# Performance work log

Hardware: AMD Instinct MI355X
Metric: run time of the kernel (lower is better)

Reference implementation:

```python
import jax, jax.numpy as jnp
import numpy as np

B, H, W, C = 8, 64, 64, 512   # C = query_dim = text_dim
K = 256                        # text tokens
TOP_M = 5
EPS = 1e-5


def _ln(x, g, b):
    mu = jnp.mean(x, axis=-1, keepdims=True)
    var = jnp.var(x, axis=-1, keepdims=True)
    return (x - mu) / jnp.sqrt(var + EPS) * g + b


def setup_inputs() -> dict:
    key = jax.random.key(0)
    ks = jax.random.split(key, 10)
    s = 0.02
    return {
        "visual": jax.random.normal(ks[0], (B, H, W, C), jnp.float32),
        "text": jax.random.normal(ks[1], (B, K, C), jnp.float32),
        "g1": jnp.ones((C,), jnp.float32), "b1": jnp.zeros((C,), jnp.float32),
        "g2": jnp.ones((C,), jnp.float32), "b2": jnp.zeros((C,), jnp.float32),
        "Wq": jax.random.normal(ks[2], (C, C), jnp.float32) * s,   # query_dim -> text_dim
        "Wv": jax.random.normal(ks[3], (C, C), jnp.float32) * s,   # text_dim -> query_dim
        "logit_scale": jnp.asarray(np.log(1.0 / 0.07), jnp.float32),
        "Wg": jax.random.normal(ks[4], (C, 1), jnp.float32) * s,
        "bg": jnp.zeros((1,), jnp.float32),
        "W1": jax.random.normal(ks[5], (C, 4 * C), jnp.float32) * s,
        "bff1": jnp.zeros((4 * C,), jnp.float32),
        "W2": jax.random.normal(ks[6], (4 * C, C), jnp.float32) * s,
        "bff2": jnp.zeros((C,), jnp.float32),
    }


def reference(visual, text, g1, b1, g2, b2, Wq, Wv, logit_scale, Wg, bg, W1, bff1, W2, bff2):
    Bv, Hv, Wdim, Cv = visual.shape
    N = Hv * Wdim
    x = _ln(visual, g1, b1).reshape(Bv, N, Cv)           # (B,N,C) pre-LN
    q = x @ Wq                                            # (B,N,Ct)
    q = q / jnp.linalg.norm(q, axis=-1, keepdims=True)
    k = text / jnp.linalg.norm(text, axis=-1, keepdims=True)  # (B,K,Ct)
    v = text @ Wv                                         # (B,K,C)
    scale = jnp.exp(logit_scale) / jnp.sqrt(jnp.asarray(Cv, jnp.float32))
    sim = jnp.einsum('bnc,bkc->bnk', q, k) * scale        # (B,N,K)
    top_vals, top_idx = jax.lax.top_k(sim, TOP_M)         # (B,N,m)
    attn = jax.nn.softmax(top_vals, axis=-1)
    v_sel = jax.vmap(lambda vb, ib: vb[ib])(v, top_idx)   # (B,N,m,C) gather
    aligned = jnp.einsum('bnm,bnmc->bnc', attn, v_sel)    # weighted sum
    gate = jax.nn.sigmoid(x @ Wg + bg)                    # (B,N,1)
    aligned = aligned * gate
    y = x + aligned                                        # residual
    y = _ln(y, g2, b2)
    h = jax.nn.gelu(y @ W1 + bff1, approximate=False)
    y = y + (h @ W2 + bff2)
    return y.reshape(Bv, Hv, Wdim, Cv)
```

## Files before the change

kernel.cpp:

```cpp
#include <hip/hip_runtime.h>
#include <hip/hip_bf16.h>

typedef unsigned short u16;
typedef float f32x4 __attribute__((ext_vector_type(4)));
typedef short bf16x8 __attribute__((ext_vector_type(8)));

#define DEV __device__ __forceinline__

DEV float btof(u16 u) { return __uint_as_float(((unsigned)u) << 16); }
DEV u16 f2b(float f) {
  unsigned u = __float_as_uint(f);
  return (u16)((u + 0x7fffu + ((u >> 16) & 1u)) >> 16);
}
DEV void gld16(const void* g, void* l) {
  __builtin_amdgcn_global_load_lds(
      (const __attribute__((address_space(1))) void*)g,
      (__attribute__((address_space(3))) void*)l, 16, 0, 0);
}
DEV float gelu_fast(float x) {
  float xx = x * x;
  float u = x * fmaf(xx, 0.0356774081f, 0.7978845608f);
  u = fminf(fmaxf(u, -15.f), 15.f);
  float e = __expf(-2.0f * u);
  float d = 1.0f + e;
  float r; asm("v_rcp_f32 %0, %1" : "=v"(r) : "v"(d));
  float t = (1.0f - e) * r;
  return 0.5f * x * (1.0f + t);
}

template <int EPI>
__global__ __launch_bounds__(512, 2) void gemm256(
    const u16* __restrict__ A, long lda, const u16* __restrict__ B, long ldb,
    void* __restrict__ Cv, long ldc, int K, long sA, long sB, long sC,
    const float* __restrict__ aux1, const void* __restrict__ aux2)
{
  __shared__ u16 lds[2][32768];
  const int tid = threadIdx.x;
  const int lane = tid & 63, wid = tid >> 6;
  const int wm = wid >> 2, wn = wid & 3;
  const int qr = lane >> 4, qc = lane & 15;

  const int gx = gridDim.x, gy = gridDim.y;
  const int nwg = gx * gy * (int)gridDim.z;
  const int orig = blockIdx.x + gx * (blockIdx.y + gy * blockIdx.z);
  const int nid = (orig & 7) * (nwg >> 3) + (orig >> 3);
  const int bx = nid % gx;
  const int rem1 = nid / gx;
  const int by = rem1 % gy;
  const long z = rem1 / gy;

  const long m0 = (long)by << 8, n0 = (long)bx << 8;
  const u16* Ab = A + z * sA;
  const u16* Bb = B + z * sB;
  const int T = K >> 6;

  f32x4 acc[8][4];
#pragma unroll
  for (int m = 0; m < 8; ++m)
#pragma unroll
    for (int n = 0; n < 4; ++n) acc[m][n] = (f32x4){0.f, 0.f, 0.f, 0.f};

  const int c0 = wid * 128 + lane, c1 = c0 + 64;
  const int r0 = c0 >> 2, r1 = c1 >> 2;
  const int k0off = ((c0 & 3) ^ ((r0 >> 1) & 3)) << 3;
  const int k1off = ((c1 & 3) ^ ((r1 >> 1) & 3)) << 3;
  const u16* pa0 = Ab + (m0 + r0) * lda + k0off;
  const u16* pa1 = Ab + (m0 + r1) * lda + k1off;
  const u16* pb0 = Bb + (n0 + r0) * ldb + k0off;
  const u16* pb1 = Bb + (n0 + r1) * ldb + k1off;
  const int e0 = c0 * 8, e1 = c1 * 8;

  const int swz = (qr ^ ((qc >> 1) & 3)) << 3;

  auto ldA = [&](bf16x8* dst, int bsel, int kh, int mh) {
#pragma unroll
    for (int mm = 0; mm < 4; ++mm) {
      const int rr = wm * 128 + (mh * 4 + mm) * 16 + qc;
      dst[mm] = *(const bf16x8*)&lds[bsel][kh * 16384 + rr * 32 + swz];
    }
  };
  auto ldB = [&](bf16x8* dst, int bsel, int kh) {
#pragma unroll
    for (int n = 0; n < 4; ++n) {
      const int rr = wn * 64 + n * 16 + qc;
      dst[n] = *(const bf16x8*)&lds[bsel][kh * 16384 + 8192 + rr * 32 + swz];
    }
  };

  gld16(pa0, &lds[0][e0]);           gld16(pa1, &lds[0][e1]);
  gld16(pb0, &lds[0][8192 + e0]);    gld16(pb1, &lds[0][8192 + e1]);
  gld16(pa0 + 32, &lds[0][16384 + e0]); gld16(pa1 + 32, &lds[0][16384 + e1]);
  gld16(pb0 + 32, &lds[0][24576 + e0]); gld16(pb1 + 32, &lds[0][24576 + e1]);
  pa0 += 64; pa1 += 64; pb0 += 64; pb1 += 64;

#define MFMAQ(MB) \
    __builtin_amdgcn_s_setprio(1); \
    _Pragma("unroll") \
    for (int mm = 0; mm < 4; ++mm) \
      _Pragma("unroll") \
      for (int n = 0; n < 4; ++n) \
        acc[MB + mm][n] = __builtin_amdgcn_mfma_f32_16x16x32_bf16( \
            a4[mm], b4[n], acc[MB + mm][n], 0, 0, 0); \
    __builtin_amdgcn_s_setprio(0);

#define TILE(BUF, PF, SO) { \
    bf16x8 a4[4], b4[4]; \
     \
    asm volatile("s_waitcnt vmcnt(4)" ::: "memory"); \
    __builtin_amdgcn_s_barrier(); \
    ldA(a4, BUF, 0, 0); ldB(b4, BUF, 0); \
    if (PF) { gld16(pa0 + (SO), &lds[BUF ^ 1][e0]); \
              gld16(pa1 + (SO), &lds[BUF ^ 1][e1]); } \
    MFMAQ(0) \
    asm volatile("s_waitcnt lgkmcnt(0)" ::: "memory"); \
     \
    __builtin_amdgcn_s_barrier(); \
    ldA(a4, BUF, 0, 1); \
    if (PF) { gld16(pb0 + (SO), &lds[BUF ^ 1][8192 + e0]); \
              gld16(pb1 + (SO), &lds[BUF ^ 1][8192 + e1]); } \
    MFMAQ(4) \
    asm volatile("s_waitcnt lgkmcnt(0)" ::: "memory"); \
     \
    if (PF) { asm volatile("s_waitcnt vmcnt(4)" ::: "memory"); } \
    else    { asm volatile("s_waitcnt vmcnt(0)" ::: "memory"); } \
    __builtin_amdgcn_s_barrier(); \
    ldA(a4, BUF, 1, 0); ldB(b4, BUF, 1); \
    if (PF) { gld16(pa0 + (SO) + 32, &lds[BUF ^ 1][16384 + e0]); \
              gld16(pa1 + (SO) + 32, &lds[BUF ^ 1][16384 + e1]); } \
    MFMAQ(0) \
    asm volatile("s_waitcnt lgkmcnt(0)" ::: "memory"); \
     \
    __builtin_amdgcn_s_barrier(); \
    ldA(a4, BUF, 1, 1); \
    if (PF) { gld16(pb0 + (SO) + 32, &lds[BUF ^ 1][24576 + e0]); \
              gld16(pb1 + (SO) + 32, &lds[BUF ^ 1][24576 + e1]); } \
    MFMAQ(4) \
    asm volatile("s_waitcnt lgkmcnt(0)" ::: "memory"); }

  for (int t2 = 0; t2 < T; t2 += 2) {
    TILE(0, true, 0)
    TILE(1, (t2 + 2 < T), 64)
    pa0 += 128; pa1 += 128; pb0 += 128; pb1 += 128;
  }
#undef TILE
#undef MFMAQ

  if constexpr (EPI == 6) {
    float* rsc2 = (float*)Cv;
#pragma unroll
    for (int m = 0; m < 8; ++m)
#pragma unroll
      for (int j = 0; j < 4; ++j) {
        float s = 0.f;
#pragma unroll
        for (int n = 0; n < 4; ++n) { float t2 = acc[m][n][j]; s = fmaf(t2, t2, s); }
        s += __shfl_xor(s, 1); s += __shfl_xor(s, 2);
        s += __shfl_xor(s, 4); s += __shfl_xor(s, 8);
        if (qc == 0)
          atomicAdd(rsc2 + (m0 + wm * 128 + m * 16 + qr * 4 + j), s);
      }
  } else {
#pragma unroll
    for (int m = 0; m < 8; ++m) {
#pragma unroll
      for (int n = 0; n < 4; ++n) {
        const long row0 = m0 + wm * 128 + m * 16 + qr * 4;
        const long col = n0 + wn * 64 + n * 16 + qc;
#pragma unroll
        for (int j = 0; j < 4; ++j) {
          const long idx = z * sC + (row0 + j) * ldc + col;
          float val = acc[m][n][j];
          if constexpr (EPI == 0) ((float*)Cv)[idx] = val;
          else if constexpr (EPI == 4)
            ((u16*)Cv)[idx] = f2b(gelu_fast(val + aux1[col]));
          else if constexpr (EPI == 5) {
            float r = btof(((const u16*)aux2)[idx]);
            ((float*)Cv)[idx] = val + aux1[col] + r;
          }
        }
      }
    }
  }
}

template <int EPI>
__global__ __launch_bounds__(256) void gemm_bt(
    const u16* __restrict__ A, long lda, const u16* __restrict__ B, long ldb,
    void* __restrict__ Cv, long ldc, int K)
{
  const int tid = threadIdx.x;
  const int lane = tid & 63, wv = tid >> 6;
  const int wr = wv >> 1, wc = wv & 1;
  const int m0 = blockIdx.y << 7, n0 = blockIdx.x << 7;

  __shared__ u16 lsA[128 * 64];
  __shared__ u16 lsB[128 * 64];

  f32x4 acc[4][4];
#pragma unroll
  for (int m = 0; m < 4; ++m)
#pragma unroll
    for (int n = 0; n < 4; ++n) acc[m][n] = (f32x4){0.f, 0.f, 0.f, 0.f};

  const int srow = tid >> 3;
  const int scol = (tid & 7) << 3;
  const int qr = lane >> 4, qc = lane & 15;

  for (int k0 = 0; k0 < K; k0 += 64) {
#pragma unroll
    for (int p = 0; p < 4; ++p) {
      gld16(A + (long)(m0 + (p << 5) + srow) * lda + k0 + scol,
            &lsA[(p * 4 + wv) * 512]);
      gld16(B + (long)(n0 + (p << 5) + srow) * ldb + k0 + scol,
            &lsB[(p * 4 + wv) * 512]);
    }
    __syncthreads();
#pragma unroll
    for (int kk = 0; kk < 64; kk += 32) {
      bf16x8 af[4], bfr[4];
#pragma unroll
      for (int m = 0; m < 4; ++m)
        af[m] = *(const bf16x8*)&lsA[(wr * 64 + m * 16 + qc) * 64 + kk + qr * 8];
#pragma unroll
      for (int n = 0; n < 4; ++n)
        bfr[n] = *(const bf16x8*)&lsB[(wc * 64 + n * 16 + qc) * 64 + kk + qr * 8];
#pragma unroll
      for (int m = 0; m < 4; ++m)
#pragma unroll
        for (int n = 0; n < 4; ++n)
          acc[m][n] = __builtin_amdgcn_mfma_f32_16x16x32_bf16(af[m], bfr[n],
                                                              acc[m][n], 0, 0, 0);
    }
    __syncthreads();
  }

#pragma unroll
  for (int m = 0; m < 4; ++m) {
#pragma unroll
    for (int n = 0; n < 4; ++n) {
      const int row0 = m0 + wr * 64 + m * 16 + qr * 4;
      const int col = n0 + wc * 64 + n * 16 + qc;
#pragma unroll
      for (int j = 0; j < 4; ++j) {
        const long idx = (long)(row0 + j) * ldc + col;
        if constexpr (EPI == 3) ((u16*)Cv)[idx] = f2b(acc[m][n][j]);
      }
    }
  }
}

__global__ __launch_bounds__(256) void transpose_bf16(
    const float* __restrict__ src, u16* __restrict__ dst, int R, int C)
{
  __shared__ float t[64][65];
  const int c0 = blockIdx.x * 64, r0 = blockIdx.y * 64;
  for (int j = threadIdx.y; j < 64; j += 4)
    t[j][threadIdx.x] = src[(long)(r0 + j) * C + c0 + threadIdx.x];
  __syncthreads();
  for (int j = threadIdx.y; j < 64; j += 4)
    dst[(long)(c0 + j) * R + r0 + threadIdx.x] = f2b(t[threadIdx.x][j]);
}

__global__ __launch_bounds__(256) void transpose_f32(
    const float* __restrict__ src, float* __restrict__ dst, int R, int C,
    long sS, long sD)
{
  __shared__ float t[64][65];
  const int c0 = blockIdx.x * 64, r0 = blockIdx.y * 64;
  const long z = blockIdx.z;
  for (int j = threadIdx.y; j < 64; j += 4)
    t[j][threadIdx.x] = src[z * sS + (long)(r0 + j) * C + c0 + threadIdx.x];
  __syncthreads();
  for (int j = threadIdx.y; j < 64; j += 4)
    dst[z * sD + (long)(c0 + j) * R + r0 + threadIdx.x] = t[threadIdx.x][j];
}

__global__ __launch_bounds__(256) void ln1_kernel(
    const float* __restrict__ vis, const float* __restrict__ g1,
    const float* __restrict__ b1, const float* __restrict__ Wg,
    const float* __restrict__ bg, u16* __restrict__ x3,
    u16* __restrict__ xr2, float* __restrict__ gate)
{
  const int lane = threadIdx.x & 63, wv = threadIdx.x >> 6;
  const long row = (long)blockIdx.x * 4 + wv;
  const float* src = vis + row * 512 + lane * 8;
  float v[8];
  *(float4*)&v[0] = *(const float4*)src;
  *(float4*)&v[4] = *(const float4*)(src + 4);
  float s = 0.f, sq = 0.f;
#pragma unroll
  for (int j = 0; j < 8; ++j) { s += v[j]; sq += v[j] * v[j]; }
#pragma unroll
  for (int off = 32; off; off >>= 1) { s += __shfl_xor(s, off); sq += __shfl_xor(sq, off); }
  const float mu = s * (1.f / 512.f);
  const float var = sq * (1.f / 512.f) - mu * mu;
  const float rstd = 1.0f / sqrtf(var + 1e-5f);

  float g1r[8], b1r[8], wgr[8];
  *(float4*)&g1r[0] = *(const float4*)(g1 + lane * 8);
  *(float4*)&g1r[4] = *(const float4*)(g1 + lane * 8 + 4);
  *(float4*)&b1r[0] = *(const float4*)(b1 + lane * 8);
  *(float4*)&b1r[4] = *(const float4*)(b1 + lane * 8 + 4);
  *(float4*)&wgr[0] = *(const float4*)(Wg + lane * 8);
  *(float4*)&wgr[4] = *(const float4*)(Wg + lane * 8 + 4);

  bf16x8 p0, p1, p2;
  float gd = 0.f;
#pragma unroll
  for (int j = 0; j < 8; ++j) {
    float d = (v[j] - mu) * rstd * g1r[j] + b1r[j];
    gd += d * wgr[j];
    u16 h0 = f2b(d);        float r1 = d - btof(h0);
    u16 h1 = f2b(r1);       float r2 = r1 - btof(h1);
    u16 h2 = f2b(r2);
    p0[j] = (short)h0; p1[j] = (short)h1; p2[j] = (short)h2;
  }
#pragma unroll
  for (int off = 32; off; off >>= 1) gd += __shfl_xor(gd, off);
  if (lane == 0) gate[row] = 1.0f / (1.0f + __expf(-(gd + bg[0])));

  u16* dst = x3 + row * 1536 + lane * 8;
  *(bf16x8*)dst = p0;
  *(bf16x8*)(dst + 512) = p1;
  *(bf16x8*)(dst + 1024) = p0;
  *(bf16x8*)(xr2 + row * 512 + lane * 8) = p2;
}

__global__ __launch_bounds__(256) void knorm_kernel(
    const float* __restrict__ text, float* __restrict__ kn, u16* __restrict__ tb)
{
  const int lane = threadIdx.x & 63, wv = threadIdx.x >> 6;
  const long row = (long)blockIdx.x * 4 + wv;
  const float* src = text + row * 512 + lane * 8;
  float v[8];
  *(float4*)&v[0] = *(const float4*)src;
  *(float4*)&v[4] = *(const float4*)(src + 4);
  float sq = 0.f;
#pragma unroll
  for (int j = 0; j < 8; ++j) sq += v[j] * v[j];
#pragma unroll
  for (int off = 32; off; off >>= 1) sq += __shfl_xor(sq, off);
  const float nrm = sqrtf(sq);
  float kv[8];
  bf16x8 pt;
#pragma unroll
  for (int j = 0; j < 8; ++j) { kv[j] = v[j] / nrm; pt[j] = (short)f2b(v[j]); }
  float* kd = kn + row * 512 + lane * 8;
  *(float4*)kd = *(float4*)&kv[0];
  *(float4*)(kd + 4) = *(float4*)&kv[4];
  *(bf16x8*)(tb + row * 512 + lane * 8) = pt;
}

__global__ __launch_bounds__(256) void wtilde_kernel(
    const float* __restrict__ Wq, const float* __restrict__ kT,
    double* __restrict__ wtmp)
{
  const int c0 = blockIdx.x * 4;
  const int b = blockIdx.y;
  __shared__ float wrow[4][512];
#pragma unroll
  for (int i = 0; i < 8; ++i) {
    int idx = threadIdx.x + i * 256;
    wrow[idx >> 9][idx & 511] = Wq[(long)c0 * 512 + idx];
  }
  __syncthreads();
  const int k = threadIdx.x;
  const float* kTb = kT + (long)b * 512 * 256 + k;
  double a0 = 0, a1 = 0, a2 = 0, a3 = 0;
  for (int j = 0; j < 512; ++j) {
    double kvd = (double)kTb[(long)j * 256];
    a0 += (double)wrow[0][j] * kvd;
    a1 += (double)wrow[1][j] * kvd;
    a2 += (double)wrow[2][j] * kvd;
    a3 += (double)wrow[3][j] * kvd;
  }
  double* o = wtmp + ((long)b * 512 + c0) * 256 + k;
  o[0] = a0; o[256] = a1; o[512] = a2; o[768] = a3;
}

__global__ __launch_bounds__(256) void wtilde_split(
    const double* __restrict__ wtmp, u16* __restrict__ wA,
    double* __restrict__ wtmpT)
{
  __shared__ double t[64][65];
  const int t0 = blockIdx.x * 64, c0 = blockIdx.y * 64, b = blockIdx.z;
  const double* s = wtmp + (long)b * 512 * 256;
  for (int j = threadIdx.y; j < 64; j += 4)
    t[j][threadIdx.x] = s[(long)(c0 + j) * 256 + t0 + threadIdx.x];
  __syncthreads();
  for (int j = threadIdx.y; j < 64; j += 4) {
    double wv = t[threadIdx.x][j];
    u16 h0 = f2b((float)wv);  double r1 = wv - (double)btof(h0);
    u16 h1 = f2b((float)r1);
    const long kb = (long)b * 256 + t0 + j;
    const int c = c0 + threadIdx.x;
    wA[kb * 1536 + c] = h0;
    wA[kb * 1536 + 512 + c] = h0;
    wA[kb * 1536 + 1024 + c] = h1;
    wtmpT[kb * 512 + c] = wv;
  }
}

__global__ __launch_bounds__(256) void qfinish_kernel(
    const float* __restrict__ rsc2, const float* __restrict__ ls,
    float* __restrict__ rsc)
{
  const int i = blockIdx.x * 256 + threadIdx.x;
  rsc[i] = __expf(ls[0]) * 0.044194173824159223f * rsqrtf(rsc2[i]);
}

__global__ __launch_bounds__(256) void topk_fuse(
    const float* __restrict__ sim, const u16* __restrict__ v,
    const u16* __restrict__ x3, const u16* __restrict__ xr2,
    const float* __restrict__ gate, const double* __restrict__ wtmpT,
    const float* __restrict__ rsc, const float* __restrict__ g2,
    const float* __restrict__ b2, u16* __restrict__ yb)
{
  const int lane = threadIdx.x & 63, wv = threadIdx.x >> 6;
  const long row = (long)blockIdx.x * 4 + wv;
  const int b = (int)(row >> 12);

  const u16* xr = x3 + row * 1536 + lane * 8;
  bf16x8 a0 = *(const bf16x8*)xr;
  bf16x8 a1 = *(const bf16x8*)(xr + 512);
  float xv[8];
#pragma unroll
  for (int j = 0; j < 8; ++j) xv[j] = btof((u16)a0[j]) + btof((u16)a1[j]);

  float4 sv = *(const float4*)(sim + row * 256 + lane * 4);
  float vals[4] = {sv.x, sv.y, sv.z, sv.w};
  float topv[8]; int topi[8];
#pragma unroll
  for (int m = 0; m < 8; ++m) {
    float bv = vals[0]; int bl = 0;
    if (vals[1] > bv) { bv = vals[1]; bl = 1; }
    if (vals[2] > bv) { bv = vals[2]; bl = 2; }
    if (vals[3] > bv) { bv = vals[3]; bl = 3; }
    int bi = lane * 4 + bl;
#pragma unroll
    for (int off = 32; off; off >>= 1) {
      float ov = __shfl_xor(bv, off);
      int oi = __shfl_xor(bi, off);
      if (ov > bv || (ov == bv && oi < bi)) { bv = ov; bi = oi; }
    }
    topv[m] = bv; topi[m] = bi;
    if ((bi >> 2) == lane) {
      int tt = bi & 3;
      if (tt == 0) vals[0] = -INFINITY; else if (tt == 1) vals[1] = -INFINITY;
      else if (tt == 2) vals[2] = -INFINITY; else vals[3] = -INFINITY;
    }
  }

  if (topv[4] - topv[5] < 2e-4f) {
    bf16x8 a2 = *(const bf16x8*)(xr2 + row * 512 + lane * 8);
    double xd[8];
#pragma unroll
    for (int j = 0; j < 8; ++j)
      xd[j] = (double)btof((u16)a0[j]) + (double)btof((u16)a1[j]) +
              (double)btof((u16)a2[j]);
    double cv[8]; int ti[8];
#pragma unroll
    for (int m = 0; m < 8; ++m) {
      const double* wp = wtmpT + ((long)b * 256 + topi[m]) * 512 + lane * 8;
      double a = 0.0;
#pragma unroll
      for (int j = 0; j < 8; ++j) a += xd[j] * wp[j];
#pragma unroll
      for (int off = 32; off; off >>= 1) a += __shfl_xor(a, off);
      cv[m] = a; ti[m] = topi[m];
    }
#define CE(i, jj) { \
    bool sw = (cv[jj] > cv[i]) || (cv[jj] == cv[i] && ti[jj] < ti[i]); \
    double tv = cv[i]; int tix = ti[i]; \
    cv[i] = sw ? cv[jj] : cv[i];  ti[i] = sw ? ti[jj] : ti[i]; \
    cv[jj] = sw ? tv : cv[jj];    ti[jj] = sw ? tix : ti[jj]; }
    CE(0,1) CE(2,3) CE(4,5) CE(6,7)
    CE(0,2) CE(1,3) CE(4,6) CE(5,7)
    CE(1,2) CE(5,6)
    CE(0,4) CE(1,5) CE(2,6) CE(3,7)
    CE(2,4) CE(3,5)
    CE(1,2) CE(3,4) CE(5,6)
#undef CE
#pragma unroll
    for (int m = 0; m < 5; ++m) { topv[m] = (float)cv[m]; topi[m] = ti[m]; }
  }

  const float rs = rsc[row];
  float e[5], se = 0.f;
#pragma unroll
  for (int m = 0; m < 5; ++m) {
    e[m] = __expf((topv[m] - topv[0]) * rs); se += e[m];
  }
  const float inv = 1.0f / se;
  const float g = gate[row];

  float acc8[8] = {0, 0, 0, 0, 0, 0, 0, 0};
#pragma unroll
  for (int m = 0; m < 5; ++m) {
    const u16* vr = v + ((long)b * 256 + topi[m]) * 512 + lane * 8;
    bf16x8 vv = *(const bf16x8*)vr;
    float wgt = e[m] * inv;
#pragma unroll
    for (int j = 0; j < 8; ++j) acc8[j] += wgt * btof((u16)vv[j]);
  }

  float y8[8]; float s = 0.f, sq = 0.f;
#pragma unroll
  for (int j = 0; j < 8; ++j) {
    y8[j] = xv[j] + acc8[j] * g;
    s += y8[j]; sq += y8[j] * y8[j];
  }
#pragma unroll
  for (int off = 32; off; off >>= 1) { s += __shfl_xor(s, off); sq += __shfl_xor(sq, off); }
  const float mu = s * (1.f / 512.f);
  const float var = sq * (1.f / 512.f) - mu * mu;
  const float rstd = 1.0f / sqrtf(var + 1e-5f);

  float g2r[8], b2r[8];
  *(float4*)&g2r[0] = *(const float4*)(g2 + lane * 8);
  *(float4*)&g2r[4] = *(const float4*)(g2 + lane * 8 + 4);
  *(float4*)&b2r[0] = *(const float4*)(b2 + lane * 8);
  *(float4*)&b2r[4] = *(const float4*)(b2 + lane * 8 + 4);
  bf16x8 outp;
#pragma unroll
  for (int j = 0; j < 8; ++j)
    outp[j] = (short)f2b((y8[j] - mu) * rstd * g2r[j] + b2r[j]);
  *(bf16x8*)(yb + row * 512 + lane * 8) = outp;
}

extern "C" void kernel_launch(void* const* d_in, const int* in_sizes, int n_in,
                              void* d_out, int out_size, void* d_ws,
                              size_t ws_size, hipStream_t stream)
{
  const float* vis  = (const float*)d_in[0];
  const float* text = (const float*)d_in[1];
  const float* g1   = (const float*)d_in[2];
  const float* b1   = (const float*)d_in[3];
  const float* g2   = (const float*)d_in[4];
  const float* b2   = (const float*)d_in[5];
  const float* Wq   = (const float*)d_in[6];
  const float* Wv   = (const float*)d_in[7];
  const float* ls   = (const float*)d_in[8];
  const float* Wg   = (const float*)d_in[9];
  const float* bg   = (const float*)d_in[10];
  const float* W1   = (const float*)d_in[11];
  const float* bff1 = (const float*)d_in[12];
  const float* W2   = (const float*)d_in[13];
  const float* bff2 = (const float*)d_in[14];
  (void)in_sizes; (void)n_in; (void)out_size; (void)ws_size;

  char* w = (char*)d_ws;
  auto alloc = [&](size_t bytes) {
    char* p = w; w += (bytes + 255) & ~(size_t)255; return p;
  };
  u16* x3 = (u16*)alloc(134217728);
  u16* h = x3;
  char* gap = (char*)x3 + 100663296;
  double* wtmp = (double*)gap;
  double* wtmpT = (double*)(gap + 8388608);
  u16* wA = (u16*)(gap + 16777216);
  float* sim = (float*)alloc(33554432);
  u16* yb = (u16*)alloc(33554432);
  u16* xr2 = (u16*)alloc(33554432);
  float* kn = (float*)alloc(4194304);
  float* kT = (float*)alloc(4194304);
  u16* tb = (u16*)alloc(2097152);
  u16* vb = (u16*)alloc(2097152);
  u16* WqT = (u16*)alloc(524288);
  u16* WvT = (u16*)alloc(524288);
  u16* W1T = (u16*)alloc(2097152);
  u16* W2T = (u16*)alloc(2097152);
  float* gate = (float*)alloc(131072);
  float* rsc = (float*)alloc(131072);
  float* rsc2 = (float*)alloc(131072);

  dim3 b256(256), b512(512), bT(64, 4);

  transpose_bf16<<<dim3(8, 8), bT, 0, stream>>>(Wq, WqT, 512, 512);
  transpose_bf16<<<dim3(8, 8), bT, 0, stream>>>(Wv, WvT, 512, 512);
  transpose_bf16<<<dim3(32, 8), bT, 0, stream>>>(W1, W1T, 512, 2048);
  transpose_bf16<<<dim3(8, 32), bT, 0, stream>>>(W2, W2T, 2048, 512);

  ln1_kernel<<<8192, b256, 0, stream>>>(vis, g1, b1, Wg, bg, x3, xr2, gate);
  knorm_kernel<<<512, b256, 0, stream>>>(text, kn, tb);
  transpose_f32<<<dim3(8, 4, 8), bT, 0, stream>>>(kn, kT, 256, 512,
                                                  256L * 512, 256L * 512);
  wtilde_kernel<<<dim3(128, 8), b256, 0, stream>>>(Wq, kT, wtmp);
  wtilde_split<<<dim3(4, 8, 8), bT, 0, stream>>>(wtmp, wA, wtmpT);

  hipMemsetAsync(rsc2, 0, 131072, stream);
  gemm256<6><<<dim3(2, 128, 1), b512, 0, stream>>>(x3, 1536, WqT, 512, rsc2,
                                                   1, 512, 0, 0, 0, nullptr,
                                                   nullptr);
  qfinish_kernel<<<128, b256, 0, stream>>>(rsc2, ls, rsc);

  gemm_bt<3><<<dim3(4, 16, 1), b256, 0, stream>>>(tb, 512, WvT, 512, vb, 512,
                                                  512);

  gemm256<0><<<dim3(1, 16, 8), b512, 0, stream>>>(
      x3, 1536, wA, 1536, sim, 256, 1536, 4096L * 1536, 256L * 1536,
      4096L * 256, nullptr, nullptr);

  topk_fuse<<<8192, b256, 0, stream>>>(sim, vb, x3, xr2, gate, wtmpT, rsc, g2,
                                       b2, yb);

  gemm256<4><<<dim3(8, 128, 1), b512, 0, stream>>>(yb, 512, W1T, 512, h, 2048,
                                                   512, 0, 0, 0, bff1,
                                                   nullptr);
  gemm256<5><<<dim3(2, 128, 1), b512, 0, stream>>>(h, 2048, W2T, 2048, d_out,
                                                   512, 2048, 0, 0, 0, bff2,
                                                   yb);
}
```

Baseline: 433.3 us.

## Restructure GEMM main loop barriers, relax launch bounds, simplify GELU approximation

Reorders the GEMM inner pipeline so that LDS fragment reads and global prefetches are issued before a barrier, then waits on lgkmcnt and runs the MFMA block, with a second barrier after each MFMA quarter. The initial tile wait is hoisted before the loop. The intent is better overlap of LDS reads with global loads, at the cost of twice as many barriers. It also changes launch bounds from 2 to 1 blocks per CU, giving the compiler more registers but possibly lowering occupancy. GELU is rewritten as a sigmoid-form tanh approximation using raw v_exp and v_rcp with no clamping, which may return NaN or Inf for large inputs.

```diff
diff --git a/kernel.cpp b/kernel.cpp
--- a/kernel.cpp
+++ b/kernel.cpp
@@ -19,17 +19,14 @@
 }
 DEV float gelu_fast(float x) {
   float xx = x * x;
-  float u = x * fmaf(xx, 0.0356774081f, 0.7978845608f);
-  u = fminf(fmaxf(u, -15.f), 15.f);
-  float e = __expf(-2.0f * u);
-  float d = 1.0f + e;
-  float r; asm("v_rcp_f32 %0, %1" : "=v"(r) : "v"(d));
-  float t = (1.0f - e) * r;
-  return 0.5f * x * (1.0f + t);
+  float p = fmaf(xx, -0.10294357f, -2.3022077f);
+  float e; asm("v_exp_f32 %0, %1" : "=v"(e) : "v"(p * x));
+  float r; asm("v_rcp_f32 %0, %1" : "=v"(r) : "v"(1.0f + e));
+  return x * r;
 }
 
 template <int EPI>
-__global__ __launch_bounds__(512, 2) void gemm256(
+__global__ __launch_bounds__(512, 1) void gemm256(
     const u16* __restrict__ A, long lda, const u16* __restrict__ B, long ldb,
     void* __restrict__ Cv, long ldc, int K, long sA, long sB, long sC,
     const float* __restrict__ aux1, const void* __restrict__ aux2)
@@ -87,11 +84,13 @@
     }
   };
 
-  gld16(pa0, &lds[0][e0]);           gld16(pa1, &lds[0][e1]);
-  gld16(pb0, &lds[0][8192 + e0]);    gld16(pb1, &lds[0][8192 + e1]);
+  gld16(pa0, &lds[0][e0]);            gld16(pa1, &lds[0][e1]);
+  gld16(pb0, &lds[0][8192 + e0]);     gld16(pb1, &lds[0][8192 + e1]);
   gld16(pa0 + 32, &lds[0][16384 + e0]); gld16(pa1 + 32, &lds[0][16384 + e1]);
   gld16(pb0 + 32, &lds[0][24576 + e0]); gld16(pb1 + 32, &lds[0][24576 + e1]);
   pa0 += 64; pa1 += 64; pb0 += 64; pb1 += 64;
+  asm volatile("s_waitcnt vmcnt(4)" ::: "memory");
+  __builtin_amdgcn_s_barrier();
 
 #define MFMAQ(MB) \
     __builtin_amdgcn_s_setprio(1); \
@@ -103,46 +102,50 @@
             a4[mm], b4[n], acc[MB + mm][n], 0, 0, 0); \
     __builtin_amdgcn_s_setprio(0);
 
-#define TILE(BUF, PF, SO) { \
+#define TILE64(BUF, PF, SO) { \
     bf16x8 a4[4], b4[4]; \
      \
-    asm volatile("s_waitcnt vmcnt(4)" ::: "memory"); \
-    __builtin_amdgcn_s_barrier(); \
     ldA(a4, BUF, 0, 0); ldB(b4, BUF, 0); \
     if (PF) { gld16(pa0 + (SO), &lds[BUF ^ 1][e0]); \
               gld16(pa1 + (SO), &lds[BUF ^ 1][e1]); } \
+    __builtin_amdgcn_s_barrier(); \
+    asm volatile("s_waitcnt lgkmcnt(0)" ::: "memory"); \
     MFMAQ(0) \
-    asm volatile("s_waitcnt lgkmcnt(0)" ::: "memory"); \
+    __builtin_amdgcn_s_barrier(); \
      \
-    __builtin_amdgcn_s_barrier(); \
     ldA(a4, BUF, 0, 1); \
     if (PF) { gld16(pb0 + (SO), &lds[BUF ^ 1][8192 + e0]); \
-              gld16(pb1 + (SO), &lds[BUF ^ 1][8192 + e1]); } \
-    MFMAQ(4) \
-    asm volatile("s_waitcnt lgkmcnt(0)" ::: "memory"); \
-     \
-    if (PF) { asm volatile("s_waitcnt vmcnt(4)" ::: "memory"); } \
+              gld16(pb1 + (SO), &lds[BUF ^ 1][8192 + e1]); \
+              asm volatile("s_waitcnt vmcnt(4)" ::: "memory"); } \
     else    { asm volatile("s_waitcnt vmcnt(0)" ::: "memory"); } \
     __builtin_amdgcn_s_barrier(); \
+    asm volatile("s_waitcnt lgkmcnt(0)" ::: "memory"); \
+    MFMAQ(4) \
+    __builtin_amdgcn_s_barrier(); \
+     \
     ldA(a4, BUF, 1, 0); ldB(b4, BUF, 1); \
     if (PF) { gld16(pa0 + (SO) + 32, &lds[BUF ^ 1][16384 + e0]); \
               gld16(pa1 + (SO) + 32, &lds[BUF ^ 1][16384 + e1]); } \
+    __builtin_amdgcn_s_barrier(); \
+    asm volatile("s_waitcnt lgkmcnt(0)" ::: "memory"); \
     MFMAQ(0) \
-    asm volatile("s_waitcnt lgkmcnt(0)" ::: "memory"); \
+    __builtin_amdgcn_s_barrier(); \
      \
-    __builtin_amdgcn_s_barrier(); \
     ldA(a4, BUF, 1, 1); \
     if (PF) { gld16(pb0 + (SO) + 32, &lds[BUF ^ 1][24576 + e0]); \
-              gld16(pb1 + (SO) + 32, &lds[BUF ^ 1][24576 + e1]); } \
+              gld16(pb1 + (SO) + 32, &lds[BUF ^ 1][24576 + e1]); \
+              asm volatile("s_waitcnt vmcnt(4)" ::: "memory"); } \
+    __builtin_amdgcn_s_barrier(); \
+    asm volatile("s_waitcnt lgkmcnt(0)" ::: "memory"); \
     MFMAQ(4) \
-    asm volatile("s_waitcnt lgkmcnt(0)" ::: "memory"); }
+    __builtin_amdgcn_s_barrier(); }
 
   for (int t2 = 0; t2 < T; t2 += 2) {
-    TILE(0, true, 0)
-    TILE(1, (t2 + 2 < T), 64)
+    TILE64(0, true, 0)
+    TILE64(1, (t2 + 2 < T), 64)
     pa0 += 128; pa1 += 128; pb0 += 128; pb1 += 128;
   }
-#undef TILE
+#undef TILE64
 #undef MFMAQ
 
   if constexpr (EPI == 6) {
```

New measurement: 451.9 us. 1.04x slower.
